# Optimization experiments

Measured on AMD Instinct MI355X. Metric: run time of the kernel, lower is better.

The kernel has to match this reference:

```python
import jax, jax.numpy as jnp
import numpy as np
import math

B, T, C = 1, 4096, 1024
N_HEAD = 16
HEAD_DIM = C // N_HEAD


def _rotate_every_two(x):
    x1 = x[..., ::2]
    x2 = x[..., 1::2]
    return jnp.stack((-x2, x1), axis=-1).reshape(x.shape)


def setup_inputs() -> dict:
    key = jax.random.key(0)
    k1, k2, k3 = jax.random.split(key, 3)
    s = 0.02
    return {
        "x": jax.random.normal(k1, (B, T, C), dtype=jnp.float32),
        "Wqkv": jax.random.normal(k2, (C, 3 * C), dtype=jnp.float32) * s,
        "bqkv": jnp.zeros((3 * C,), dtype=jnp.float32),
        "Wproj": jax.random.normal(k3, (C, C), dtype=jnp.float32) * s,
        "bproj": jnp.zeros((C,), dtype=jnp.float32),
    }


def reference(x, Wqkv, bqkv, Wproj, bproj):
    b, t, c = x.shape
    qkv = x @ Wqkv + bqkv                      # [B,T,3C]
    q, k, v = jnp.split(qkv, 3, axis=2)
    # [B,H,T,D]
    q = q.reshape(b, t, N_HEAD, HEAD_DIM).transpose(0, 2, 1, 3)
    k = k.reshape(b, t, N_HEAD, HEAD_DIM).transpose(0, 2, 1, 3)
    v = v.reshape(b, t, N_HEAD, HEAD_DIM).transpose(0, 2, 1, 3)

    # RoPE (as in source: emb = cat(freqs, freqs), rotate_every_two interleaved)
    inv_freq = 1.0 / (10000.0 ** (jnp.arange(0, HEAD_DIM, 2, dtype=jnp.float32) / HEAD_DIM))
    pos = jnp.arange(t, dtype=jnp.float32)
    freqs = pos[:, None] * inv_freq[None, :]          # [T, D/2]
    emb = jnp.concatenate((freqs, freqs), axis=-1)    # [T, D]
    cos = jnp.cos(emb)[None, None, :, :]
    sin = jnp.sin(emb)[None, None, :, :]
    q = q * cos + _rotate_every_two(q) * sin
    k = k * cos + _rotate_every_two(k) * sin

    att = jnp.einsum('bhqd,bhkd->bhqk', q, k) / math.sqrt(HEAD_DIM)
    causal = jnp.tril(jnp.ones((t, t), dtype=bool))
    att = jnp.where(causal[None, None], att, -jnp.inf)
    att = jax.nn.softmax(att, axis=-1)
    y = jnp.einsum('bhqk,bhkd->bhqd', att, v)         # [B,H,T,D]
    y = y.transpose(0, 2, 1, 3).reshape(b, t, c)
    return y @ Wproj + bproj
```

## Files before the change

### kernel.cpp

```cpp
#include <hip/hip_runtime.h>
#include <hip/hip_bf16.h>
#include <cstdint>
#include <cstddef>

constexpr int TSEQ = 4096;
constexpr int CDIM = 1024;
constexpr int NHEAD = 16;
constexpr int HDIM = 64;
constexpr float QSCALE = 0.125f * 1.4426950408889634f;

using bf16 = __hip_bfloat16;
typedef __bf16 bf16x8 __attribute__((ext_vector_type(8)));
typedef float floatx4 __attribute__((ext_vector_type(4)));

__device__ inline uint32_t cvt_pk_bf16(float a, float b) {
  uint32_t r;
  asm("v_cvt_pk_bf16_f32 %0, %1, %2" : "=v"(r) : "v"(a), "v"(b));
  return r;
}
__device__ inline floatx4 vadd4(floatx4 a, floatx4 b) {
  floatx4 r;
  r[0] = a[0] + b[0]; r[1] = a[1] + b[1];
  r[2] = a[2] + b[2]; r[3] = a[3] + b[3];
  return r;
}
__device__ inline void gload_lds16(const bf16* g, bf16* l) {
  __builtin_amdgcn_global_load_lds(
      (const __attribute__((address_space(1))) void*)g,
      (__attribute__((address_space(3))) void*)l, 16, 0, 0);
}

__global__ __launch_bounds__(256) void f32_to_bf16(
    const float4* __restrict__ in, uint64_t* __restrict__ out, int n4) {
  const int i = blockIdx.x * 256 + threadIdx.x;
  if (i < n4) {
    const float4 v = in[i];
    union { bf16 h[4]; uint64_t u; } p;
    p.h[0] = __float2bfloat16(v.x);
    p.h[1] = __float2bfloat16(v.y);
    p.h[2] = __float2bfloat16(v.z);
    p.h[3] = __float2bfloat16(v.w);
    out[i] = p.u;
  }
}

__global__ __launch_bounds__(256) void rope_table(float* __restrict__ tab) {
  const int i = blockIdx.x * 256 + threadIdx.x;
  const int t = i >> 5, j = i & 31;
  const float invf = exp2f((float)j * (-2.0f / 64.0f) * 13.287712379549449f);
  float sn, cs;
  sincosf((float)t * invf, &sn, &cs);
  tab[t * 64 + j] = cs;
  tab[t * 64 + 32 + j] = sn;
}

__global__ __launch_bounds__(256) void transpose_f32_bf16(
    const float* __restrict__ in, bf16* __restrict__ out, int R, int C) {
  __shared__ float tile[32][33];
  const int c0 = blockIdx.x * 32, r0 = blockIdx.y * 32;
  const int tx = threadIdx.x, ty = threadIdx.y;
#pragma unroll
  for (int i = 0; i < 32; i += 8)
    tile[ty + i][tx] = in[(size_t)(r0 + ty + i) * C + c0 + tx];
  __syncthreads();
#pragma unroll
  for (int i = 0; i < 32; i += 8)
    out[(size_t)(c0 + ty + i) * R + r0 + tx] = __float2bfloat16(tile[tx][ty + i]);
}

template <int MODE>
__global__ __launch_bounds__(256) void gemm_bt(
    const bf16* __restrict__ A, const bf16* __restrict__ Bt,
    const float* __restrict__ bias, const float* __restrict__ tab,
    float* __restrict__ Cout,
    bf16* __restrict__ Qh, bf16* __restrict__ Kh, bf16* __restrict__ Vt,
    int M, int N, int K) {
  __shared__ __align__(16) bf16 smem[4 * 64 * 72];
  bf16* As = smem;
  bf16* Bs = smem + 128 * 64;
  const int tid = threadIdx.x;
  const int m0 = blockIdx.y * 128, n0 = blockIdx.x * 128;
  const int wave = tid >> 6, lane = tid & 63;
  const int l15 = lane & 15, quad = lane >> 4;
  const int wm = (wave >> 1) * 64, wn = (wave & 1) * 64;

  const floatx4 fzero = {0.f, 0.f, 0.f, 0.f};
  floatx4 acc[4][4];
#pragma unroll
  for (int mi = 0; mi < 4; mi++)
#pragma unroll
    for (int ni = 0; ni < 4; ni++) acc[mi][ni] = fzero;

  const int gr = lane >> 3;
  const int gcs = ((lane & 7) ^ gr) << 3;
  const bf16* Ag = A + (size_t)(m0 + wave * 32 + gr) * K + gcs;
  const bf16* Bg = Bt + (size_t)(n0 + wave * 32 + gr) * K + gcs;
  bf16* Asw = As + wave * 32 * 64;
  bf16* Bsw = Bs + wave * 32 * 64;

  const int x7f = l15 & 7;
  const int af0 = (quad ^ x7f) << 3;
  const int af1 = ((4 + quad) ^ x7f) << 3;

  for (int k0 = 0; k0 < K; k0 += 64) {
    __syncthreads();
#pragma unroll
    for (int j = 0; j < 4; j++) {
      gload_lds16(Ag + (size_t)j * 8 * K + k0, Asw + j * 512);
      gload_lds16(Bg + (size_t)j * 8 * K + k0, Bsw + j * 512);
    }
    __syncthreads();

    bf16x8 a[4][2], b[4][2];
#pragma unroll
    for (int mi = 0; mi < 4; mi++) {
      const bf16* ar = As + (wm + mi * 16 + l15) * 64;
      a[mi][0] = *(const bf16x8*)(ar + af0);
      a[mi][1] = *(const bf16x8*)(ar + af1);
    }
#pragma unroll
    for (int ni = 0; ni < 4; ni++) {
      const bf16* br = Bs + (wn + ni * 16 + l15) * 64;
      b[ni][0] = *(const bf16x8*)(br + af0);
      b[ni][1] = *(const bf16x8*)(br + af1);
    }
#pragma unroll
    for (int kk = 0; kk < 2; kk++)
#pragma unroll
      for (int mi = 0; mi < 4; mi++)
#pragma unroll
        for (int ni = 0; ni < 4; ni++)
          acc[mi][ni] = __builtin_amdgcn_mfma_f32_16x16x32_bf16(
              a[mi][kk], b[ni][kk], acc[mi][ni], 0, 0, 0);
  }

  __syncthreads();

  if (MODE == 1) {
    bf16* ep = smem + (size_t)wave * (64 * 72);
    const int cbase = n0 + wn;
    const int sec = cbase >> 10;
    const int hh = (cbase & 1023) >> 6;
    if (sec == 2) {
#pragma unroll
      for (int ni = 0; ni < 4; ni++) {
        const int d = ni * 16 + l15;
        const float bv = bias[cbase + d];
#pragma unroll
        for (int mi = 0; mi < 4; mi++) {
          const uint32_t lo =
              cvt_pk_bf16(acc[mi][ni][0] + bv, acc[mi][ni][1] + bv);
          const uint32_t hi =
              cvt_pk_bf16(acc[mi][ni][2] + bv, acc[mi][ni][3] + bv);
          *(uint64_t*)(ep + (size_t)d * 72 + mi * 16 + quad * 4) =
              (uint64_t)lo | ((uint64_t)hi << 32);
        }
      }
      __asm__ __volatile__("" ::: "memory");
#pragma unroll
      for (int it = 0; it < 8; it++) {
        const int dr = it * 8 + (lane >> 3);
        const int t8 = (lane & 7) * 8;
        const bf16x8 vv = *(const bf16x8*)(ep + (size_t)dr * 72 + t8);
        *(bf16x8*)(Vt + ((size_t)hh * HDIM + dr) * TSEQ + m0 + wm + t8) = vv;
      }
    } else {
      bf16* dst = (sec == 0) ? Qh : Kh;
      const float postscale = (sec == 0) ? QSCALE : 1.0f;
#pragma unroll
      for (int ni = 0; ni < 4; ni++) {
        const int c = ni * 16 + l15;
        const float bv = bias[cbase + c];
        const int j = c & 31;
#pragma unroll
        for (int mi = 0; mi < 4; mi++) {
#pragma unroll
          for (int r = 0; r < 4; r++) {
            const int t = m0 + wm + mi * 16 + quad * 4 + r;
            const float v = acc[mi][ni][r] + bv;
            const float partner = __shfl_xor(v, 1, 64);
            const float cs = tab[t * 64 + j];
            const float sn = tab[t * 64 + 32 + j];
            const float res =
                (v * cs + ((c & 1) ? partner : -partner) * sn) * postscale;
            ep[(size_t)(mi * 16 + quad * 4 + r) * 72 + c] =
                __float2bfloat16(res);
          }
        }
      }
      __asm__ __volatile__("" ::: "memory");
#pragma unroll
      for (int it = 0; it < 8; it++) {
        const int row = it * 8 + (lane >> 3);
        const int c8 = (lane & 7) * 8;
        const bf16x8 vv = *(const bf16x8*)(ep + (size_t)row * 72 + c8);
        *(bf16x8*)(dst + ((size_t)hh * TSEQ + m0 + wm + row) * HDIM + c8) = vv;
      }
    }
  } else {
    float* ep32 = (float*)smem + (size_t)wave * (32 * 68);
    float bvv[4];
#pragma unroll
    for (int ni = 0; ni < 4; ni++) bvv[ni] = bias[n0 + wn + ni * 16 + l15];
#pragma unroll
    for (int half = 0; half < 2; half++) {
      if (half) __asm__ __volatile__("" ::: "memory");
#pragma unroll
      for (int ni = 0; ni < 4; ni++)
#pragma unroll
        for (int mi2 = 0; mi2 < 2; mi2++)
#pragma unroll
          for (int r = 0; r < 4; r++)
            ep32[(size_t)(mi2 * 16 + quad * 4 + r) * 68 + ni * 16 + l15] =
                acc[half * 2 + mi2][ni][r] + bvv[ni];
      __asm__ __volatile__("" ::: "memory");
#pragma unroll
      for (int it = 0; it < 8; it++) {
        const int row = it * 4 + (lane >> 4);
        const float4 vv = *(const float4*)(ep32 + (size_t)row * 68 + l15 * 4);
        *(float4*)(Cout + (size_t)(m0 + wm + half * 32 + row) * N + n0 + wn +
                   l15 * 4) = vv;
      }
    }
  }
}

__global__ __launch_bounds__(256) void attn_kernel(
    const bf16* __restrict__ Qh, const bf16* __restrict__ Kh,
    const bf16* __restrict__ Vt, bf16* __restrict__ Y) {
  const int h = blockIdx.y;
  const int p = blockIdx.x;
  const int tile_lo = p, tile_hi = 63 - p;
  const int tid = threadIdx.x;
  const int w = tid >> 6, lane = tid & 63;
  const int l15 = lane & 15, quad = lane >> 4;
  const int q_lo = tile_lo * 64 + w * 16 + l15;
  const int q_hi = tile_hi * 64 + w * 16 + l15;
  const int nkv_lo = tile_lo + 1;
  const int nkv_hi = tile_hi + 1;

  const bf16* Qb = Qh + (size_t)h * TSEQ * HDIM;
  const bf16* Kb = Kh + (size_t)h * TSEQ * HDIM;
  const bf16* Vb = Vt + (size_t)h * HDIM * TSEQ;

  __shared__ __align__(16) bf16 Ks[2][64 * 64];
  __shared__ __align__(16) bf16 Vs[2][64 * 64];
  __shared__ bf16 Plds[4][32][72];

  const int sr = tid >> 3;
  const int sc = tid & 7;
  const int sp = sc << 3;
  const int sofs = sr * 64 + ((sc ^ (sr & 7)) << 3);

  bf16x8 Rk0, Rk1, Rv0, Rv1;
  auto stage_load = [&](int kv0) {
    Rk0 = *(const bf16x8*)(Kb + (size_t)(kv0 + sr) * HDIM + sp);
    Rk1 = *(const bf16x8*)(Kb + (size_t)(kv0 + sr + 32) * HDIM + sp);
    Rv0 = *(const bf16x8*)(Vb + (size_t)sr * TSEQ + kv0 + sp);
    Rv1 = *(const bf16x8*)(Vb + (size_t)(sr + 32) * TSEQ + kv0 + sp);
  };
  auto stage_write = [&](int buf) {
    *(bf16x8*)(Ks[buf] + sofs) = Rk0;
    *(bf16x8*)(Ks[buf] + sofs + 32 * 64) = Rk1;
    *(bf16x8*)(Vs[buf] + sofs) = Rv0;
    *(bf16x8*)(Vs[buf] + sofs + 32 * 64) = Rv1;
  };

  const int x7 = l15 & 7;
  const int fofs0 = ((quad ^ x7) << 3);
  const int fofs1 = (((4 + quad) ^ x7) << 3);

  bf16x8 qf[2][2];
#pragma unroll
  for (int ks = 0; ks < 2; ks++) {
    qf[0][ks] = *(const bf16x8*)(Qb + (size_t)q_lo * HDIM + ks * 32 + quad * 8);
    qf[1][ks] = *(const bf16x8*)(Qb + (size_t)q_hi * HDIM + ks * 32 + quad * 8);
  }

  const floatx4 fzero = {0.f, 0.f, 0.f, 0.f};
  floatx4 o[2][4];
  floatx4 lacc[2] = {fzero, fzero};
#pragma unroll
  for (int qt = 0; qt < 2; qt++)
#pragma unroll
    for (int dt = 0; dt < 4; dt++) o[qt][dt] = fzero;

  auto exp_tile = [&](floatx4* s, int qrow, bool maskit, int kv0, int qt) {
    if (maskit) {
#pragma unroll
      for (int kt = 0; kt < 4; kt++)
#pragma unroll
        for (int r = 0; r < 4; r++) {
          const int kv = kv0 + kt * 16 + quad * 4 + r;
          if (kv > qrow) s[kt][r] = -1e30f;
        }
    }
#pragma unroll
    for (int kt = 0; kt < 4; kt++)
#pragma unroll
      for (int r = 0; r < 4; r++)
        s[kt][r] = __builtin_amdgcn_exp2f(s[kt][r]);
    lacc[qt] = vadd4(lacc[qt], vadd4(vadd4(s[0], s[1]), vadd4(s[2], s[3])));
#pragma unroll
    for (int kt = 0; kt < 4; kt++) {
      const uint32_t lo = cvt_pk_bf16(s[kt][0], s[kt][1]);
      const uint32_t hi = cvt_pk_bf16(s[kt][2], s[kt][3]);
      *(uint64_t*)(&Plds[w][qt * 16 + l15][kt * 16 + quad * 4]) =
          (uint64_t)lo | ((uint64_t)hi << 32);
    }
  };

  stage_load(0);
  stage_write(0);
  __syncthreads();

  int cur = 0;
  for (int kb = 0; kb < nkv_hi; kb++) {
    const int kv0 = kb * 64;
    const bool lo_on = (kb < nkv_lo);
    const bool have_next = (kb + 1 < nkv_hi);

    if (have_next) stage_load(kv0 + 64);

    floatx4 sh[4], sl[4];
#pragma unroll
    for (int kt = 0; kt < 4; kt++) { sh[kt] = fzero; sl[kt] = fzero; }
    __builtin_amdgcn_s_setprio(1);
#pragma unroll
    for (int kt = 0; kt < 4; kt++) {
      const bf16* krow = Ks[cur] + (kt * 16 + l15) * 64;
      const bf16x8 kf0 = *(const bf16x8*)(krow + fofs0);
      const bf16x8 kf1 = *(const bf16x8*)(krow + fofs1);
      sh[kt] = __builtin_amdgcn_mfma_f32_16x16x32_bf16(
          kf0, qf[1][0], sh[kt], 0, 0, 0);
      sh[kt] = __builtin_amdgcn_mfma_f32_16x16x32_bf16(
          kf1, qf[1][1], sh[kt], 0, 0, 0);
      if (lo_on) {
        sl[kt] = __builtin_amdgcn_mfma_f32_16x16x32_bf16(
            kf0, qf[0][0], sl[kt], 0, 0, 0);
        sl[kt] = __builtin_amdgcn_mfma_f32_16x16x32_bf16(
            kf1, qf[0][1], sl[kt], 0, 0, 0);
      }
    }
    __builtin_amdgcn_s_setprio(0);

    exp_tile(sh, q_hi, kb == nkv_hi - 1, kv0, 1);
    if (lo_on) exp_tile(sl, q_lo, kb == nkv_lo - 1, kv0, 0);
    __asm__ __volatile__("" ::: "memory");

    bf16x8 ph[2], pl[2];
#pragma unroll
    for (int ks = 0; ks < 2; ks++)
      ph[ks] = *(const bf16x8*)(&Plds[w][16 + l15][ks * 32 + quad * 8]);
    if (lo_on) {
#pragma unroll
      for (int ks = 0; ks < 2; ks++)
        pl[ks] = *(const bf16x8*)(&Plds[w][l15][ks * 32 + quad * 8]);
    }
    __builtin_amdgcn_s_setprio(1);
#pragma unroll
    for (int dt = 0; dt < 4; dt++) {
      const bf16* vrow = Vs[cur] + (dt * 16 + l15) * 64;
      const bf16x8 vf0 = *(const bf16x8*)(vrow + fofs0);
      const bf16x8 vf1 = *(const bf16x8*)(vrow + fofs1);
      o[1][dt] = __builtin_amdgcn_mfma_f32_16x16x32_bf16(
          vf0, ph[0], o[1][dt], 0, 0, 0);
      o[1][dt] = __builtin_amdgcn_mfma_f32_16x16x32_bf16(
          vf1, ph[1], o[1][dt], 0, 0, 0);
      if (lo_on) {
        o[0][dt] = __builtin_amdgcn_mfma_f32_16x16x32_bf16(
            vf0, pl[0], o[0][dt], 0, 0, 0);
        o[0][dt] = __builtin_amdgcn_mfma_f32_16x16x32_bf16(
            vf1, pl[1], o[0][dt], 0, 0, 0);
      }
    }
    __builtin_amdgcn_s_setprio(0);

    if (have_next) stage_write(cur ^ 1);
    __syncthreads();
    cur ^= 1;
  }

#pragma unroll
  for (int qt = 0; qt < 2; qt++) {
    const int q = (qt == 0) ? q_lo : q_hi;
    float l = (lacc[qt][0] + lacc[qt][1]) + (lacc[qt][2] + lacc[qt][3]);
    l += __shfl_xor(l, 16, 64);
    l += __shfl_xor(l, 32, 64);
    const float inv = 1.0f / l;
#pragma unroll
    for (int dt = 0; dt < 4; dt++) {
      const uint32_t lo = cvt_pk_bf16(o[qt][dt][0] * inv, o[qt][dt][1] * inv);
      const uint32_t hi = cvt_pk_bf16(o[qt][dt][2] * inv, o[qt][dt][3] * inv);
      *(uint64_t*)(Y + (size_t)q * CDIM + h * HDIM + dt * 16 + quad * 4) =
          (uint64_t)lo | ((uint64_t)hi << 32);
    }
  }
}

extern "C" void kernel_launch(void* const* d_in, const int* in_sizes, int n_in,
                              void* d_out, int out_size, void* d_ws,
                              size_t ws_size, hipStream_t stream) {
  const float* x     = (const float*)d_in[0];
  const float* Wqkv  = (const float*)d_in[1];
  const float* bqkv  = (const float*)d_in[2];
  const float* Wproj = (const float*)d_in[3];
  const float* bproj = (const float*)d_in[4];
  float* out = (float*)d_out;

  char* ws = (char*)d_ws;
  bf16* xb     = (bf16*)(ws);
  bf16* Y      = (bf16*)(ws);
  bf16* WqkvT  = (bf16*)(ws + (8ull  << 20));
  bf16* WprojT = (bf16*)(ws + (14ull << 20));
  float* tab   = (float*)(ws + (14ull << 20));
  bf16* Qh     = (bf16*)(ws + (16ull << 20));
  bf16* Kh     = (bf16*)(ws + (24ull << 20));
  bf16* Vt     = (bf16*)(ws + (32ull << 20));

  f32_to_bf16<<<dim3(4096), 256, 0, stream>>>((const float4*)x, (uint64_t*)xb,
                                              TSEQ * CDIM / 4);
  transpose_f32_bf16<<<dim3(96, 32), dim3(32, 8), 0, stream>>>(
      Wqkv, WqkvT, CDIM, 3 * CDIM);
  rope_table<<<dim3(TSEQ * 32 / 256), 256, 0, stream>>>(tab);
  gemm_bt<1><<<dim3(24, 32), 256, 0, stream>>>(
      xb, WqkvT, bqkv, tab, (float*)nullptr, Qh, Kh, Vt, TSEQ, 3 * CDIM, CDIM);
  transpose_f32_bf16<<<dim3(32, 32), dim3(32, 8), 0, stream>>>(
      Wproj, WprojT, CDIM, CDIM);
  attn_kernel<<<dim3(32, 16), 256, 0, stream>>>(Qh, Kh, Vt, Y);
  gemm_bt<0><<<dim3(8, 32), 256, 0, stream>>>(
      Y, WprojT, bproj, (float*)nullptr, out, (bf16*)nullptr, (bf16*)nullptr,
      (bf16*)nullptr, TSEQ, CDIM, CDIM);
}
```

Measured before the change: 247.0 us.

## Split attention KV range across two blocks with atomic bf16 accumulation

Each causal tile-pair is split into two blocks covering disjoint KV ranges, doubling the attention grid to improve CU occupancy. Partial unnormalized outputs are accumulated into a zeroed bf16 buffer with packed atomic adds and row sums via float atomics, then a separate kernel normalizes. This adds memsets, an extra pass, atomic traffic and extra bf16 rounding error.

```diff
diff --git a/kernel.cpp b/kernel.cpp
--- a/kernel.cpp
+++ b/kernel.cpp
@@ -28,6 +28,10 @@
   __builtin_amdgcn_global_load_lds(
       (const __attribute__((address_space(1))) void*)g,
       (__attribute__((address_space(3))) void*)l, 16, 0, 0);
+}
+__device__ inline void atomic_pk_add_bf16(bf16* addr, uint32_t data) {
+  asm volatile("global_atomic_pk_add_bf16 %0, %1, off"
+               :: "v"(addr), "v"(data) : "memory");
 }
 
 __global__ __launch_bounds__(256) void f32_to_bf16(
@@ -227,9 +231,11 @@
 
 __global__ __launch_bounds__(256) void attn_kernel(
     const bf16* __restrict__ Qh, const bf16* __restrict__ Kh,
-    const bf16* __restrict__ Vt, bf16* __restrict__ Y) {
+    const bf16* __restrict__ Vt, bf16* __restrict__ Yacc,
+    float* __restrict__ Lacc) {
   const int h = blockIdx.y;
-  const int p = blockIdx.x;
+  const int s = blockIdx.x;
+  const int p = s >> 1, half = s & 1;
   const int tile_lo = p, tile_hi = 63 - p;
   const int tid = threadIdx.x;
   const int w = tid >> 6, lane = tid & 63;
@@ -238,6 +244,10 @@
   const int q_hi = tile_hi * 64 + w * 16 + l15;
   const int nkv_lo = tile_lo + 1;
   const int nkv_hi = tile_hi + 1;
+  const int mid = (nkv_lo >= 17) ? 17 : (33 - nkv_lo);
+  const int beg = half ? mid : 0;
+  const int end = half ? nkv_hi : mid;
+  const bool any_lo = beg < nkv_lo;
 
   const bf16* Qb = Qh + (size_t)h * TSEQ * HDIM;
   const bf16* Kb = Kh + (size_t)h * TSEQ * HDIM;
@@ -285,40 +295,40 @@
 #pragma unroll
     for (int dt = 0; dt < 4; dt++) o[qt][dt] = fzero;
 
-  auto exp_tile = [&](floatx4* s, int qrow, bool maskit, int kv0, int qt) {
+  auto exp_tile = [&](floatx4* s2, int qrow, bool maskit, int kv0, int qt) {
     if (maskit) {
 #pragma unroll
       for (int kt = 0; kt < 4; kt++)
 #pragma unroll
         for (int r = 0; r < 4; r++) {
           const int kv = kv0 + kt * 16 + quad * 4 + r;
-          if (kv > qrow) s[kt][r] = -1e30f;
+          if (kv > qrow) s2[kt][r] = -1e30f;
         }
     }
 #pragma unroll
     for (int kt = 0; kt < 4; kt++)
 #pragma unroll
       for (int r = 0; r < 4; r++)
-        s[kt][r] = __builtin_amdgcn_exp2f(s[kt][r]);
-    lacc[qt] = vadd4(lacc[qt], vadd4(vadd4(s[0], s[1]), vadd4(s[2], s[3])));
+        s2[kt][r] = __builtin_amdgcn_exp2f(s2[kt][r]);
+    lacc[qt] = vadd4(lacc[qt], vadd4(vadd4(s2[0], s2[1]), vadd4(s2[2], s2[3])));
 #pragma unroll
     for (int kt = 0; kt < 4; kt++) {
-      const uint32_t lo = cvt_pk_bf16(s[kt][0], s[kt][1]);
-      const uint32_t hi = cvt_pk_bf16(s[kt][2], s[kt][3]);
+      const uint32_t lo = cvt_pk_bf16(s2[kt][0], s2[kt][1]);
+      const uint32_t hi = cvt_pk_bf16(s2[kt][2], s2[kt][3]);
       *(uint64_t*)(&Plds[w][qt * 16 + l15][kt * 16 + quad * 4]) =
           (uint64_t)lo | ((uint64_t)hi << 32);
     }
   };
 
-  stage_load(0);
+  stage_load(beg * 64);
   stage_write(0);
   __syncthreads();
 
   int cur = 0;
-  for (int kb = 0; kb < nkv_hi; kb++) {
+  for (int kb = beg; kb < end; kb++) {
     const int kv0 = kb * 64;
     const bool lo_on = (kb < nkv_lo);
-    const bool have_next = (kb + 1 < nkv_hi);
+    const bool have_next = (kb + 1 < end);
 
     if (have_next) stage_load(kv0 + 64);
 
@@ -383,19 +393,38 @@
 
 #pragma unroll
   for (int qt = 0; qt < 2; qt++) {
+    if (qt == 0 && !any_lo) continue;
     const int q = (qt == 0) ? q_lo : q_hi;
     float l = (lacc[qt][0] + lacc[qt][1]) + (lacc[qt][2] + lacc[qt][3]);
     l += __shfl_xor(l, 16, 64);
     l += __shfl_xor(l, 32, 64);
-    const float inv = 1.0f / l;
+    if (quad == 0) atomicAdd(&Lacc[(size_t)h * TSEQ + q], l);
 #pragma unroll
     for (int dt = 0; dt < 4; dt++) {
-      const uint32_t lo = cvt_pk_bf16(o[qt][dt][0] * inv, o[qt][dt][1] * inv);
-      const uint32_t hi = cvt_pk_bf16(o[qt][dt][2] * inv, o[qt][dt][3] * inv);
-      *(uint64_t*)(Y + (size_t)q * CDIM + h * HDIM + dt * 16 + quad * 4) =
-          (uint64_t)lo | ((uint64_t)hi << 32);
-    }
-  }
+      const uint32_t lo = cvt_pk_bf16(o[qt][dt][0], o[qt][dt][1]);
+      const uint32_t hi = cvt_pk_bf16(o[qt][dt][2], o[qt][dt][3]);
+      bf16* dst = Yacc + (size_t)q * CDIM + h * HDIM + dt * 16 + quad * 4;
+      atomic_pk_add_bf16(dst, lo);
+      atomic_pk_add_bf16(dst + 2, hi);
+    }
+  }
+}
+
+__global__ __launch_bounds__(256) void attn_norm(
+    bf16* __restrict__ Y, const float* __restrict__ L) {
+  const int i = blockIdx.x * 256 + threadIdx.x;
+  const int q = i >> 7;
+  const int c8 = (i & 127) << 3;
+  const float inv = 1.0f / L[(size_t)(c8 >> 6) * TSEQ + q];
+  union { bf16x8 v; bf16 e[8]; uint32_t u[4]; } x;
+  x.v = *(const bf16x8*)(Y + (size_t)q * CDIM + c8);
+#pragma unroll
+  for (int j = 0; j < 4; j++) {
+    const float a = __bfloat162float(x.e[2 * j]) * inv;
+    const float b = __bfloat162float(x.e[2 * j + 1]) * inv;
+    x.u[j] = cvt_pk_bf16(a, b);
+  }
+  *(bf16x8*)(Y + (size_t)q * CDIM + c8) = x.v;
 }
 
 extern "C" void kernel_launch(void* const* d_in, const int* in_sizes, int n_in,
@@ -412,6 +441,7 @@
   bf16* xb     = (bf16*)(ws);
   bf16* Y      = (bf16*)(ws);
   bf16* WqkvT  = (bf16*)(ws + (8ull  << 20));
+  float* Lacc  = (float*)(ws + (8ull << 20));
   bf16* WprojT = (bf16*)(ws + (14ull << 20));
   float* tab   = (float*)(ws + (14ull << 20));
   bf16* Qh     = (bf16*)(ws + (16ull << 20));
@@ -427,7 +457,10 @@
       xb, WqkvT, bqkv, tab, (float*)nullptr, Qh, Kh, Vt, TSEQ, 3 * CDIM, CDIM);
   transpose_f32_bf16<<<dim3(32, 32), dim3(32, 8), 0, stream>>>(
       Wproj, WprojT, CDIM, CDIM);
-  attn_kernel<<<dim3(32, 16), 256, 0, stream>>>(Qh, Kh, Vt, Y);
+  hipMemsetAsync(Y, 0, (size_t)TSEQ * CDIM * sizeof(bf16), stream);
+  hipMemsetAsync(Lacc, 0, (size_t)NHEAD * TSEQ * sizeof(float), stream);
+  attn_kernel<<<dim3(64, 16), 256, 0, stream>>>(Qh, Kh, Vt, Y, Lacc);
+  attn_norm<<<dim3(TSEQ * CDIM / 8 / 256), 256, 0, stream>>>(Y, Lacc);
   gemm_bt<0><<<dim3(8, 32), 256, 0, stream>>>(
       Y, WprojT, bproj, (float*)nullptr, out, (bf16*)nullptr, (bf16*)nullptr,
       (bf16*)nullptr, TSEQ, CDIM, CDIM);
```

New measurement: 274.4 us. 1.11x slower.
